# Optimization experiments

Measured on AMD Instinct MI355X. Metric: run time of the kernel, lower is better.

## Reference

```python
import jax, jax.numpy as jnp
import numpy as np

WIDTH = [768, 2048, 2048, 512]
GRID = 8
BATCH = 4096


def _init_coeffs(key, outdim, inputdim, gridsize):
    # smooth_initialization=True: randn / (sqrt(inputdim) * (k+1)^2)
    grid_norm = (jnp.arange(gridsize, dtype=jnp.float32) + 1.0) ** 2  # (grid,)
    c = jax.random.normal(key, (2, outdim, inputdim, gridsize), dtype=jnp.float32)
    return c / (np.sqrt(inputdim).astype(np.float32) * grid_norm)


def setup_inputs() -> dict:
    key = jax.random.key(0)
    ks = jax.random.split(key, 1 + len(WIDTH) - 1)
    x = jax.random.normal(ks[0], (BATCH, WIDTH[0]), dtype=jnp.float32)
    inp = {"x": x}
    for li, (din, dout) in enumerate(zip(WIDTH[:-1], WIDTH[1:])):
        inp[f"C{li + 1}"] = _init_coeffs(ks[li + 1], dout, din, GRID)
        inp[f"b{li + 1}"] = jnp.zeros((1, dout), dtype=jnp.float32)
    return inp


def _kan_layer(x, C, b):
    # x: (B, in); C: (2, out, in, grid); b: (1, out)
    g = C.shape[-1]
    k = jnp.arange(1, g + 1, dtype=x.dtype)  # (grid,)
    ang = x[..., None] * k  # (B, in, grid)
    feats = jnp.stack([jnp.cos(ang), jnp.sin(ang)], axis=0)  # (2, B, in, grid)
    # GEMM-like contraction over (in, grid) and the cos/sin axis
    y = jnp.einsum("dbik,djik->bj", feats, C) + b  # (B, out)
    return y


def reference(x, C1, b1, C2, b2, C3, b3):
    y = _kan_layer(x, C1, b1)
    y = _kan_layer(y, C2, b2)
    y = _kan_layer(y, C3, b3)
    return y
```

## Files before the change

kernel.cpp:

```cpp
#include <hip/hip_runtime.h>

#define BATCH 4096

typedef __attribute__((ext_vector_type(8))) short bf16x8;
typedef __attribute__((ext_vector_type(4))) float f32x4;

__device__ __forceinline__ unsigned short f2bf(float f) {
    union { float f; unsigned u; } v; v.f = f;
    unsigned r = v.u + 0x7fffu + ((v.u >> 16) & 1u);
    return (unsigned short)(r >> 16);
}
__device__ __forceinline__ unsigned packbf(float a, float b) {
    return (unsigned)f2bf(a) | ((unsigned)f2bf(b) << 16);
}

__device__ __forceinline__ void feats16(float x, unsigned o[8]) {
    float c1 = __cosf(x), s1 = __sinf(x);
    float cs[8], sn[8];
    cs[0] = c1; sn[0] = s1;
    #pragma unroll
    for (int k = 1; k < 8; ++k) {
        cs[k] = c1 * cs[k-1] - s1 * sn[k-1];
        sn[k] = s1 * cs[k-1] + c1 * sn[k-1];
    }
    #pragma unroll
    for (int k = 0; k < 4; ++k) {
        o[k]     = packbf(cs[2*k], cs[2*k+1]);
        o[4 + k] = packbf(sn[2*k], sn[2*k+1]);
    }
}

__device__ __forceinline__ void gload_lds16(const void* g, void* l) {
    __builtin_amdgcn_global_load_lds(
        (__attribute__((address_space(1))) void*)(g),
        (__attribute__((address_space(3))) void*)(l), 16, 0, 0);
}


template <int IN, int OUT>
__global__ void conv_C(const float* __restrict__ C, unsigned short* __restrict__ B) {
    const int i = blockIdx.x * 256 + threadIdx.x;
    const int j = blockIdx.y;
    const float* c0 = C + ((size_t)j * IN + i) * 8;
    const float* c1 = c0 + (size_t)OUT * IN * 8;
    const float4 a0 = *(const float4*)c0;
    const float4 a1 = *(const float4*)(c0 + 4);
    const float4 s0 = *(const float4*)c1;
    const float4 s1 = *(const float4*)(c1 + 4);
    unsigned short* dst = B + ((size_t)j * IN + i) * 16;
    *(uint4*)dst       = make_uint4(packbf(a0.x, a0.y), packbf(a0.z, a0.w),
                                    packbf(a1.x, a1.y), packbf(a1.z, a1.w));
    *(uint4*)(dst + 8) = make_uint4(packbf(s0.x, s0.y), packbf(s0.z, s0.w),
                                    packbf(s1.x, s1.y), packbf(s1.z, s1.w));
}

__global__ void feats_x_kernel(const float* __restrict__ x, unsigned short* __restrict__ A) {
    const size_t idx = (size_t)blockIdx.x * 256 + threadIdx.x;
    unsigned o[8];
    feats16(x[idx], o);
    unsigned short* dst = A + idx * 16;
    *(uint4*)dst       = make_uint4(o[0], o[1], o[2], o[3]);
    *(uint4*)(dst + 8) = make_uint4(o[4], o[5], o[6], o[7]);
}

template <int N, int KSPLIT>
__global__ void reduce_feats(const float* __restrict__ P, const float* __restrict__ bias,
                             unsigned short* __restrict__ A) {
    const size_t idx = (size_t)blockIdx.x * 256 + threadIdx.x;
    float s = P[idx];
    #pragma unroll
    for (int z = 1; z < KSPLIT; ++z) s += P[(size_t)z * BATCH * N + idx];
    s += bias[idx % N];
    unsigned o[8];
    feats16(s, o);
    unsigned short* dst = A + idx * 16;
    *(uint4*)dst       = make_uint4(o[0], o[1], o[2], o[3]);
    *(uint4*)(dst + 8) = make_uint4(o[4], o[5], o[6], o[7]);
}

template <int N, int KSPLIT>
__global__ void reduce_out(const float* __restrict__ P, const float* __restrict__ bias,
                           float* __restrict__ out) {
    const size_t idx = ((size_t)blockIdx.x * 256 + threadIdx.x) * 4;
    const int j = (int)(idx % N);
    float4 s = *(const float4*)(P + idx);
    #pragma unroll
    for (int z = 1; z < KSPLIT; ++z) {
        const float4 v = *(const float4*)(P + (size_t)z * BATCH * N + idx);
        s.x += v.x; s.y += v.y; s.z += v.z; s.w += v.w;
    }
    const float4 bv = *(const float4*)(bias + j);
    s.x += bv.x; s.y += bv.y; s.z += bv.z; s.w += bv.w;
    *(float4*)(out + idx) = s;
}

template <int K, int N, int KSPLIT>
__global__ __launch_bounds__(512, 2)
void kan_gemm(const unsigned short* __restrict__ A,
              const unsigned short* __restrict__ B,
              float* __restrict__ P)
{
    __shared__ unsigned short As[2 * 2 * 128 * 64];
    __shared__ unsigned short Bs[2 * 2 * 128 * 64];

    const int tid  = threadIdx.x;
    const int lane = tid & 63;
    const int wave = tid >> 6;
    const int wm   = wave >> 2;
    const int wn   = wave & 3;
    const int fr   = lane & 15;
    const int fq   = lane >> 4;

    constexpr int NBX = BATCH / 256;
    constexpr int NBY = N / 256;
    constexpr int NWG = NBX * NBY;
    constexpr int S   = NWG / 8;
    constexpr int CC  = (NBY >= 8) ? 8 : NBY;
    constexpr int CR  = S / CC;
    constexpr int GR  = NBX / CR;
    const int wg  = blockIdx.y * NBX + blockIdx.x;
    const int xc  = wg & 7;
    const int ci  = wg >> 3;
    const int row0 = ((xc % GR) * CR + ci % CR) * 256;
    const int col0 = ((xc / GR) * CC + ci / CR) * 256;

    constexpr int KCH = K / KSPLIT;
    const int kt0 = ((int)blockIdx.z * KCH) >> 6;
    const int nt  = KCH >> 6;

    const int srow = lane >> 3;
    const int scol = ((lane & 7) ^ srow) * 16;

    auto STA = [&](int b, int h, int kt) {
        #pragma unroll
        for (int r2 = 0; r2 < 2; ++r2)
            gload_lds16((const char*)A +
                        ((size_t)(row0 + h * 128 + r2 * 64 + wave * 8 + srow) * K + (size_t)kt * 64) * 2 + scol,
                        (char*)&As[((b * 2 + h) * 128 + r2 * 64 + wave * 8) * 64]);
    };
    auto STB = [&](int b, int h, int kt) {
        #pragma unroll
        for (int r2 = 0; r2 < 2; ++r2)
            gload_lds16((const char*)B +
                        ((size_t)(col0 + h * 128 + r2 * 64 + wave * 8 + srow) * K + (size_t)kt * 64) * 2 + scol,
                        (char*)&Bs[((b * 2 + h) * 128 + r2 * 64 + wave * 8) * 64]);
    };
    auto LDA = [&](int b, int m, int ks) -> bf16x8 {
        return *(const bf16x8*)&As[((b * 2 + wm) * 128 + m * 16 + fr) * 64 +
                                   (((ks * 4 + fq) ^ (fr & 7)) << 3)];
    };
    auto LDB = [&](int b, int n, int ks) -> bf16x8 {
        return *(const bf16x8*)&Bs[((b * 2 + (wn >> 1)) * 128 + (wn & 1) * 64 + n * 16 + fr) * 64 +
                                   (((ks * 4 + fq) ^ (fr & 7)) << 3)];
    };

    f32x4 acc[8][4] = {};

    STA(0, 0, kt0); STA(0, 1, kt0); STB(0, 0, kt0); STB(0, 1, kt0);
    STA(1, 0, kt0 + 1); STA(1, 1, kt0 + 1); STB(1, 0, kt0 + 1);
    asm volatile("s_waitcnt vmcnt(6)" ::: "memory");
    __builtin_amdgcn_s_barrier();

    #pragma unroll 1
    for (int t = 0; t < nt; ++t) {
        const int b  = t & 1;
        const int kt = kt0 + t;
        bf16x8 bF[8], aFa[8], aFb[8];

        #pragma unroll
        for (int n = 0; n < 4; ++n) { bF[n * 2] = LDB(b, n, 0); bF[n * 2 + 1] = LDB(b, n, 1); }
        #pragma unroll
        for (int mm = 0; mm < 4; ++mm) { aFa[mm * 2] = LDA(b, mm, 0); aFa[mm * 2 + 1] = LDA(b, mm, 1); }
        if (t + 1 < nt) STB(b ^ 1, 1, kt + 1);
        __builtin_amdgcn_s_barrier();
        asm volatile("s_waitcnt lgkmcnt(0)" ::: "memory");
        __builtin_amdgcn_sched_barrier(0);
        __builtin_amdgcn_s_setprio(1);
        #pragma unroll
        for (int ks = 0; ks < 2; ++ks)
            #pragma unroll
            for (int mm = 0; mm < 2; ++mm)
                #pragma unroll
                for (int n = 0; n < 4; ++n)
                    acc[mm][n] = __builtin_amdgcn_mfma_f32_16x16x32_bf16(
                        aFa[mm * 2 + ks], bF[n * 2 + ks], acc[mm][n], 0, 0, 0);
        __builtin_amdgcn_s_setprio(0);
        __builtin_amdgcn_s_barrier();

        #pragma unroll
        for (int mm = 0; mm < 4; ++mm) { aFb[mm * 2] = LDA(b, 4 + mm, 0); aFb[mm * 2 + 1] = LDA(b, 4 + mm, 1); }
        if (t + 2 < nt) STB(b, 0, kt + 2);
        __builtin_amdgcn_s_barrier();
        asm volatile("s_waitcnt lgkmcnt(0)" ::: "memory");
        __builtin_amdgcn_sched_barrier(0);
        __builtin_amdgcn_s_setprio(1);
        #pragma unroll
        for (int ks = 0; ks < 2; ++ks)
            #pragma unroll
            for (int mm = 0; mm < 2; ++mm)
                #pragma unroll
                for (int n = 0; n < 4; ++n)
                    acc[2 + mm][n] = __builtin_amdgcn_mfma_f32_16x16x32_bf16(
                        aFa[(2 + mm) * 2 + ks], bF[n * 2 + ks], acc[2 + mm][n], 0, 0, 0);
        __builtin_amdgcn_s_setprio(0);
        __builtin_amdgcn_s_barrier();

        if (t + 2 < nt) STA(b, 0, kt + 2);
        __builtin_amdgcn_s_barrier();
        __builtin_amdgcn_sched_barrier(0);
        __builtin_amdgcn_s_setprio(1);
        #pragma unroll
        for (int ks = 0; ks < 2; ++ks)
            #pragma unroll
            for (int mm = 0; mm < 2; ++mm)
                #pragma unroll
                for (int n = 0; n < 4; ++n)
                    acc[4 + mm][n] = __builtin_amdgcn_mfma_f32_16x16x32_bf16(
                        aFb[mm * 2 + ks], bF[n * 2 + ks], acc[4 + mm][n], 0, 0, 0);
        __builtin_amdgcn_s_setprio(0);
        __builtin_amdgcn_s_barrier();

        if (t + 2 < nt) {
            STA(b, 1, kt + 2);
            asm volatile("s_waitcnt vmcnt(6)" ::: "memory");
        } else {
            asm volatile("s_waitcnt vmcnt(0)" ::: "memory");
        }
        __builtin_amdgcn_s_barrier();
        __builtin_amdgcn_sched_barrier(0);
        __builtin_amdgcn_s_setprio(1);
        #pragma unroll
        for (int ks = 0; ks < 2; ++ks)
            #pragma unroll
            for (int mm = 0; mm < 2; ++mm)
                #pragma unroll
                for (int n = 0; n < 4; ++n)
                    acc[6 + mm][n] = __builtin_amdgcn_mfma_f32_16x16x32_bf16(
                        aFb[(2 + mm) * 2 + ks], bF[n * 2 + ks], acc[6 + mm][n], 0, 0, 0);
        __builtin_amdgcn_s_setprio(0);
        __builtin_amdgcn_s_barrier();
    }

    float* Pz = P + (size_t)blockIdx.z * BATCH * N;
    #pragma unroll
    for (int m = 0; m < 8; ++m) {
        const int gr0 = row0 + wm * 128 + m * 16 + fq * 4;
        #pragma unroll
        for (int n = 0; n < 4; ++n) {
            const int gc = col0 + wn * 64 + n * 16 + fr;
            #pragma unroll
            for (int q = 0; q < 4; ++q)
                Pz[(size_t)(gr0 + q) * N + gc] = acc[m][n][q];
        }
    }
}

extern "C" void kernel_launch(void* const* d_in, const int* in_sizes, int n_in,
                              void* d_out, int out_size, void* d_ws, size_t ws_size,
                              hipStream_t stream) {
    (void)in_sizes; (void)n_in; (void)ws_size; (void)out_size;
    const float* x  = (const float*)d_in[0];
    const float* C1 = (const float*)d_in[1];
    const float* b1 = (const float*)d_in[2];
    const float* C2 = (const float*)d_in[3];
    const float* b2 = (const float*)d_in[4];
    const float* C3 = (const float*)d_in[5];
    const float* b3 = (const float*)d_in[6];
    float* out = (float*)d_out;

    char* ws = (char*)d_ws;
    const size_t SZ_A1  = (size_t)4096 * 12288 * 2;
    const size_t SZ_B1  = (size_t)2048 * 12288 * 2;
    const size_t SZ_P12 = (size_t)2 * 4096 * 2048 * 4;
    const size_t SZ_A2  = (size_t)4096 * 32768 * 2;
    unsigned short* A1 = (unsigned short*)(ws);
    unsigned short* B1 = (unsigned short*)(ws + SZ_A1);
    float*          P1 = (float*)(ws + SZ_A1 + SZ_B1);
    unsigned short* A2 = (unsigned short*)(ws + SZ_A1 + SZ_B1 + SZ_P12);
    unsigned short* B2 = (unsigned short*)(ws);
    float*          P2 = (float*)(ws + SZ_A1 + SZ_B1 + SZ_P12 + SZ_A2);
    unsigned short* A3 = (unsigned short*)(ws);
    unsigned short* B3 = (unsigned short*)(ws + SZ_A2);
    float*          P3 = (float*)(ws + SZ_A2 + (size_t)512 * 32768 * 2);

    conv_C<768, 2048><<<dim3(768 / 256, 2048), 256, 0, stream>>>(C1, B1);
    feats_x_kernel<<<dim3((4096 * 768) / 256), 256, 0, stream>>>(x, A1);
    kan_gemm<12288, 2048, 2><<<dim3(16, 8, 2), 512, 0, stream>>>(A1, B1, P1);
    reduce_feats<2048, 2><<<dim3((BATCH * 2048) / 256), 256, 0, stream>>>(P1, b1, A2);

    conv_C<2048, 2048><<<dim3(2048 / 256, 2048), 256, 0, stream>>>(C2, B2);
    kan_gemm<32768, 2048, 2><<<dim3(16, 8, 2), 512, 0, stream>>>(A2, B2, P2);
    reduce_feats<2048, 2><<<dim3((BATCH * 2048) / 256), 256, 0, stream>>>(P2, b2, A3);

    conv_C<2048, 512><<<dim3(2048 / 256, 512), 256, 0, stream>>>(C3, B3);
    kan_gemm<32768, 512, 8><<<dim3(16, 2, 8), 512, 0, stream>>>(A3, B3, P3);
    reduce_out<512, 8><<<dim3((BATCH * 512 / 4) / 256), 256, 0, stream>>>(P3, b3, out);
}
```

Baseline: 1.147 ms.

## Software-pipeline LDS fragment loads across MFMA phases with partial lgkmcnt waits

Restructures the GEMM main loop so LDS fragment loads for the next phase are issued before the current MFMA phase. Partial lgkmcnt waits replace the full drains, and the first-k-slice fragments of the next tile are prefetched at the end of each tile. The loop is unrolled by two with a compile-time buffer index, and all three next-tile global stores are grouped into the last phase. The goal is to hide LDS read latency behind MFMA work. In exchange it needs more registers for carried fragments, and it assumes nt is even.

```diff
diff --git a/kernel.cpp b/kernel.cpp
--- a/kernel.cpp
+++ b/kernel.cpp
@@ -94,6 +94,9 @@
     *(float4*)(out + idx) = s;
 }
 
+struct IC0 { static constexpr int value = 0; };
+struct IC1 { static constexpr int value = 1; };
+
 template <int K, int N, int KSPLIT>
 __global__ __launch_bounds__(512, 2)
 void kan_gemm(const unsigned short* __restrict__ A,
@@ -155,90 +158,105 @@
     };
 
     f32x4 acc[8][4] = {};
+    bf16x8 cB0[4], cA0[4];
 
     STA(0, 0, kt0); STA(0, 1, kt0); STB(0, 0, kt0); STB(0, 1, kt0);
-    STA(1, 0, kt0 + 1); STA(1, 1, kt0 + 1); STB(1, 0, kt0 + 1);
+    STB(1, 0, kt0 + 1); STA(1, 0, kt0 + 1); STA(1, 1, kt0 + 1);
     asm volatile("s_waitcnt vmcnt(6)" ::: "memory");
+    __builtin_amdgcn_sched_barrier(0);
     __builtin_amdgcn_s_barrier();
-
-    #pragma unroll 1
-    for (int t = 0; t < nt; ++t) {
-        const int b  = t & 1;
+    #pragma unroll
+    for (int n = 0; n < 4; ++n) cB0[n] = LDB(0, n, 0);
+    #pragma unroll
+    for (int m = 0; m < 4; ++m) cA0[m] = LDA(0, m, 0);
+    __builtin_amdgcn_sched_barrier(0);
+
+    auto tile = [&](auto bc, int t) {
+        constexpr int b = decltype(bc)::value;
         const int kt = kt0 + t;
-        bf16x8 bF[8], aFa[8], aFb[8];
-
-        #pragma unroll
-        for (int n = 0; n < 4; ++n) { bF[n * 2] = LDB(b, n, 0); bF[n * 2 + 1] = LDB(b, n, 1); }
-        #pragma unroll
-        for (int mm = 0; mm < 4; ++mm) { aFa[mm * 2] = LDA(b, mm, 0); aFa[mm * 2 + 1] = LDA(b, mm, 1); }
+        bf16x8 vA01[4], vB1[4], vA10[4], vA11[4];
+
+        #pragma unroll
+        for (int m = 0; m < 4; ++m) vA01[m] = LDA(b, 4 + m, 0);
+        #pragma unroll
+        for (int n = 0; n < 4; ++n) vB1[n] = LDB(b, n, 1);
         if (t + 1 < nt) STB(b ^ 1, 1, kt + 1);
+        __builtin_amdgcn_sched_barrier(0);
+        __builtin_amdgcn_s_barrier();
+        asm volatile("s_waitcnt lgkmcnt(8)" ::: "memory");
+        __builtin_amdgcn_sched_barrier(0);
+        __builtin_amdgcn_s_setprio(1);
+        #pragma unroll
+        for (int m = 0; m < 4; ++m)
+            #pragma unroll
+            for (int n = 0; n < 4; ++n)
+                acc[m][n] = __builtin_amdgcn_mfma_f32_16x16x32_bf16(cA0[m], cB0[n], acc[m][n], 0, 0, 0);
+        __builtin_amdgcn_s_setprio(0);
+
+        #pragma unroll
+        for (int m = 0; m < 4; ++m) vA10[m] = LDA(b, m, 1);
+        #pragma unroll
+        for (int m = 0; m < 4; ++m) vA11[m] = LDA(b, 4 + m, 1);
+        __builtin_amdgcn_sched_barrier(0);
+        __builtin_amdgcn_s_barrier();
+        asm volatile("s_waitcnt lgkmcnt(12)" ::: "memory");
+        __builtin_amdgcn_sched_barrier(0);
+        __builtin_amdgcn_s_setprio(1);
+        #pragma unroll
+        for (int m = 0; m < 4; ++m)
+            #pragma unroll
+            for (int n = 0; n < 4; ++n)
+                acc[4 + m][n] = __builtin_amdgcn_mfma_f32_16x16x32_bf16(vA01[m], cB0[n], acc[4 + m][n], 0, 0, 0);
+        __builtin_amdgcn_s_setprio(0);
+
+        __builtin_amdgcn_sched_barrier(0);
         __builtin_amdgcn_s_barrier();
         asm volatile("s_waitcnt lgkmcnt(0)" ::: "memory");
         __builtin_amdgcn_sched_barrier(0);
         __builtin_amdgcn_s_setprio(1);
         #pragma unroll
-        for (int ks = 0; ks < 2; ++ks)
-            #pragma unroll
-            for (int mm = 0; mm < 2; ++mm)
-                #pragma unroll
-                for (int n = 0; n < 4; ++n)
-                    acc[mm][n] = __builtin_amdgcn_mfma_f32_16x16x32_bf16(
-                        aFa[mm * 2 + ks], bF[n * 2 + ks], acc[mm][n], 0, 0, 0);
+        for (int m = 0; m < 4; ++m)
+            #pragma unroll
+            for (int n = 0; n < 4; ++n)
+                acc[m][n] = __builtin_amdgcn_mfma_f32_16x16x32_bf16(vA10[m], vB1[n], acc[m][n], 0, 0, 0);
         __builtin_amdgcn_s_setprio(0);
-        __builtin_amdgcn_s_barrier();
-
-        #pragma unroll
-        for (int mm = 0; mm < 4; ++mm) { aFb[mm * 2] = LDA(b, 4 + mm, 0); aFb[mm * 2 + 1] = LDA(b, 4 + mm, 1); }
-        if (t + 2 < nt) STB(b, 0, kt + 2);
-        __builtin_amdgcn_s_barrier();
-        asm volatile("s_waitcnt lgkmcnt(0)" ::: "memory");
-        __builtin_amdgcn_sched_barrier(0);
-        __builtin_amdgcn_s_setprio(1);
-        #pragma unroll
-        for (int ks = 0; ks < 2; ++ks)
-            #pragma unroll
-            for (int mm = 0; mm < 2; ++mm)
-                #pragma unroll
-                for (int n = 0; n < 4; ++n)
-                    acc[2 + mm][n] = __builtin_amdgcn_mfma_f32_16x16x32_bf16(
-                        aFa[(2 + mm) * 2 + ks], bF[n * 2 + ks], acc[2 + mm][n], 0, 0, 0);
-        __builtin_amdgcn_s_setprio(0);
-        __builtin_amdgcn_s_barrier();
-
-        if (t + 2 < nt) STA(b, 0, kt + 2);
-        __builtin_amdgcn_s_barrier();
-        __builtin_amdgcn_sched_barrier(0);
-        __builtin_amdgcn_s_setprio(1);
-        #pragma unroll
-        for (int ks = 0; ks < 2; ++ks)
-            #pragma unroll
-            for (int mm = 0; mm < 2; ++mm)
-                #pragma unroll
-                for (int n = 0; n < 4; ++n)
-                    acc[4 + mm][n] = __builtin_amdgcn_mfma_f32_16x16x32_bf16(
-                        aFb[mm * 2 + ks], bF[n * 2 + ks], acc[4 + mm][n], 0, 0, 0);
-        __builtin_amdgcn_s_setprio(0);
+        __builtin_amdgcn_sched_barrier(0);
         __builtin_amdgcn_s_barrier();
 
         if (t + 2 < nt) {
-            STA(b, 1, kt + 2);
+            STB(b, 0, kt + 2); STA(b, 0, kt + 2); STA(b, 1, kt + 2);
             asm volatile("s_waitcnt vmcnt(6)" ::: "memory");
         } else {
             asm volatile("s_waitcnt vmcnt(0)" ::: "memory");
         }
-        __builtin_amdgcn_s_barrier();
+        __builtin_amdgcn_sched_barrier(0);
+        __builtin_amdgcn_s_barrier();
+        if (t + 1 < nt) {
+            #pragma unroll
+            for (int n = 0; n < 4; ++n) cB0[n] = LDB(b ^ 1, n, 0);
+            #pragma unroll
+            for (int m = 0; m < 4; ++m) cA0[m] = LDA(b ^ 1, m, 0);
+            __builtin_amdgcn_sched_barrier(0);
+            asm volatile("s_waitcnt lgkmcnt(8)" ::: "memory");
+        } else {
+            asm volatile("s_waitcnt lgkmcnt(0)" ::: "memory");
+        }
         __builtin_amdgcn_sched_barrier(0);
         __builtin_amdgcn_s_setprio(1);
         #pragma unroll
-        for (int ks = 0; ks < 2; ++ks)
-            #pragma unroll
-            for (int mm = 0; mm < 2; ++mm)
-                #pragma unroll
-                for (int n = 0; n < 4; ++n)
-                    acc[6 + mm][n] = __builtin_amdgcn_mfma_f32_16x16x32_bf16(
-                        aFb[(2 + mm) * 2 + ks], bF[n * 2 + ks], acc[6 + mm][n], 0, 0, 0);
+        for (int m = 0; m < 4; ++m)
+            #pragma unroll
+            for (int n = 0; n < 4; ++n)
+                acc[4 + m][n] = __builtin_amdgcn_mfma_f32_16x16x32_bf16(vA11[m], vB1[n], acc[4 + m][n], 0, 0, 0);
         __builtin_amdgcn_s_setprio(0);
-        __builtin_amdgcn_s_barrier();
+        __builtin_amdgcn_sched_barrier(0);
+        __builtin_amdgcn_s_barrier();
+    };
+
+    #pragma unroll 1
+    for (int t = 0; t < nt; t += 2) {
+        tile(IC0{}, t);
+        tile(IC1{}, t + 1);
     }
 
     float* Pz = P + (size_t)blockIdx.z * BATCH * N;
```

Result: slower. 3.355 ms (+192.6%).

## Relax GEMM LDS waits and barriers, vectorize reduce_feats by four

Applied to the files above, without the earlier changes.

The GEMM main loop drops the extra barrier after each MFMA phase. It replaces full lgkmcnt(0) waits with partial counts, so MFMAs can start while later LDS fragment reads are still in flight, and it adds sched_barriers to pin the instruction order. The reduce_feats kernel now handles four elements per thread with float4 loads and a quarter of the grid. Partial waits depend on the exact LDS instruction count and order, so any miscount or reordering could read stale fragments or race with the next buffer fill.

```diff
diff --git a/kernel.cpp b/kernel.cpp
--- a/kernel.cpp
+++ b/kernel.cpp
@@ -66,16 +66,24 @@
 template <int N, int KSPLIT>
 __global__ void reduce_feats(const float* __restrict__ P, const float* __restrict__ bias,
                              unsigned short* __restrict__ A) {
-    const size_t idx = (size_t)blockIdx.x * 256 + threadIdx.x;
-    float s = P[idx];
-    #pragma unroll
-    for (int z = 1; z < KSPLIT; ++z) s += P[(size_t)z * BATCH * N + idx];
-    s += bias[idx % N];
-    unsigned o[8];
-    feats16(s, o);
+    const size_t idx = ((size_t)blockIdx.x * 256 + threadIdx.x) * 4;
+    const int j = (int)(idx % N);
+    float4 s = *(const float4*)(P + idx);
+    #pragma unroll
+    for (int z = 1; z < KSPLIT; ++z) {
+        const float4 v = *(const float4*)(P + (size_t)z * BATCH * N + idx);
+        s.x += v.x; s.y += v.y; s.z += v.z; s.w += v.w;
+    }
+    const float4 bv = *(const float4*)(bias + j);
+    const float y[4] = { s.x + bv.x, s.y + bv.y, s.z + bv.z, s.w + bv.w };
     unsigned short* dst = A + idx * 16;
-    *(uint4*)dst       = make_uint4(o[0], o[1], o[2], o[3]);
-    *(uint4*)(dst + 8) = make_uint4(o[4], o[5], o[6], o[7]);
+    #pragma unroll
+    for (int e = 0; e < 4; ++e) {
+        unsigned o[8];
+        feats16(y[e], o);
+        *(uint4*)(dst + e * 16)     = make_uint4(o[0], o[1], o[2], o[3]);
+        *(uint4*)(dst + e * 16 + 8) = make_uint4(o[4], o[5], o[6], o[7]);
+    }
 }
 
 template <int N, int KSPLIT>
@@ -157,9 +165,10 @@
     f32x4 acc[8][4] = {};
 
     STA(0, 0, kt0); STA(0, 1, kt0); STB(0, 0, kt0); STB(0, 1, kt0);
-    STA(1, 0, kt0 + 1); STA(1, 1, kt0 + 1); STB(1, 0, kt0 + 1);
+    STB(1, 0, kt0 + 1); STA(1, 0, kt0 + 1); STA(1, 1, kt0 + 1);
     asm volatile("s_waitcnt vmcnt(6)" ::: "memory");
     __builtin_amdgcn_s_barrier();
+    __builtin_amdgcn_sched_barrier(0);
 
     #pragma unroll 1
     for (int t = 0; t < nt; ++t) {
@@ -170,10 +179,14 @@
         #pragma unroll
         for (int n = 0; n < 4; ++n) { bF[n * 2] = LDB(b, n, 0); bF[n * 2 + 1] = LDB(b, n, 1); }
         #pragma unroll
-        for (int mm = 0; mm < 4; ++mm) { aFa[mm * 2] = LDA(b, mm, 0); aFa[mm * 2 + 1] = LDA(b, mm, 1); }
+        for (int mm = 0; mm < 2; ++mm) { aFa[mm * 2] = LDA(b, mm, 0); aFa[mm * 2 + 1] = LDA(b, mm, 1); }
+        __builtin_amdgcn_sched_barrier(0);
+        #pragma unroll
+        for (int mm = 2; mm < 4; ++mm) { aFa[mm * 2] = LDA(b, mm, 0); aFa[mm * 2 + 1] = LDA(b, mm, 1); }
         if (t + 1 < nt) STB(b ^ 1, 1, kt + 1);
-        __builtin_amdgcn_s_barrier();
-        asm volatile("s_waitcnt lgkmcnt(0)" ::: "memory");
+        __builtin_amdgcn_sched_barrier(0);
+        __builtin_amdgcn_s_barrier();
+        asm volatile("s_waitcnt lgkmcnt(4)" ::: "memory");
         __builtin_amdgcn_sched_barrier(0);
         __builtin_amdgcn_s_setprio(1);
         #pragma unroll
@@ -185,13 +198,16 @@
                     acc[mm][n] = __builtin_amdgcn_mfma_f32_16x16x32_bf16(
                         aFa[mm * 2 + ks], bF[n * 2 + ks], acc[mm][n], 0, 0, 0);
         __builtin_amdgcn_s_setprio(0);
-        __builtin_amdgcn_s_barrier();
-
-        #pragma unroll
-        for (int mm = 0; mm < 4; ++mm) { aFb[mm * 2] = LDA(b, 4 + mm, 0); aFb[mm * 2 + 1] = LDA(b, 4 + mm, 1); }
+
+        #pragma unroll
+        for (int mm = 0; mm < 2; ++mm) { aFb[mm * 2] = LDA(b, 4 + mm, 0); aFb[mm * 2 + 1] = LDA(b, 4 + mm, 1); }
+        __builtin_amdgcn_sched_barrier(0);
+        #pragma unroll
+        for (int mm = 2; mm < 4; ++mm) { aFb[mm * 2] = LDA(b, 4 + mm, 0); aFb[mm * 2 + 1] = LDA(b, 4 + mm, 1); }
         if (t + 2 < nt) STB(b, 0, kt + 2);
-        __builtin_amdgcn_s_barrier();
-        asm volatile("s_waitcnt lgkmcnt(0)" ::: "memory");
+        __builtin_amdgcn_sched_barrier(0);
+        __builtin_amdgcn_s_barrier();
+        asm volatile("s_waitcnt lgkmcnt(8)" ::: "memory");
         __builtin_amdgcn_sched_barrier(0);
         __builtin_amdgcn_s_setprio(1);
         #pragma unroll
@@ -203,10 +219,11 @@
                     acc[2 + mm][n] = __builtin_amdgcn_mfma_f32_16x16x32_bf16(
                         aFa[(2 + mm) * 2 + ks], bF[n * 2 + ks], acc[2 + mm][n], 0, 0, 0);
         __builtin_amdgcn_s_setprio(0);
-        __builtin_amdgcn_s_barrier();
 
         if (t + 2 < nt) STA(b, 0, kt + 2);
-        __builtin_amdgcn_s_barrier();
+        __builtin_amdgcn_sched_barrier(0);
+        __builtin_amdgcn_s_barrier();
+        asm volatile("s_waitcnt lgkmcnt(4)" ::: "memory");
         __builtin_amdgcn_sched_barrier(0);
         __builtin_amdgcn_s_setprio(1);
         #pragma unroll
@@ -218,7 +235,6 @@
                     acc[4 + mm][n] = __builtin_amdgcn_mfma_f32_16x16x32_bf16(
                         aFb[mm * 2 + ks], bF[n * 2 + ks], acc[4 + mm][n], 0, 0, 0);
         __builtin_amdgcn_s_setprio(0);
-        __builtin_amdgcn_s_barrier();
 
         if (t + 2 < nt) {
             STA(b, 1, kt + 2);
@@ -226,7 +242,9 @@
         } else {
             asm volatile("s_waitcnt vmcnt(0)" ::: "memory");
         }
-        __builtin_amdgcn_s_barrier();
+        __builtin_amdgcn_sched_barrier(0);
+        __builtin_amdgcn_s_barrier();
+        asm volatile("s_waitcnt lgkmcnt(0)" ::: "memory");
         __builtin_amdgcn_sched_barrier(0);
         __builtin_amdgcn_s_setprio(1);
         #pragma unroll
@@ -238,6 +256,7 @@
                     acc[6 + mm][n] = __builtin_amdgcn_mfma_f32_16x16x32_bf16(
                         aFb[(2 + mm) * 2 + ks], bF[n * 2 + ks], acc[6 + mm][n], 0, 0, 0);
         __builtin_amdgcn_s_setprio(0);
+        __builtin_amdgcn_sched_barrier(0);
         __builtin_amdgcn_s_barrier();
     }
 
@@ -286,11 +305,11 @@
     conv_C<768, 2048><<<dim3(768 / 256, 2048), 256, 0, stream>>>(C1, B1);
     feats_x_kernel<<<dim3((4096 * 768) / 256), 256, 0, stream>>>(x, A1);
     kan_gemm<12288, 2048, 2><<<dim3(16, 8, 2), 512, 0, stream>>>(A1, B1, P1);
-    reduce_feats<2048, 2><<<dim3((BATCH * 2048) / 256), 256, 0, stream>>>(P1, b1, A2);
+    reduce_feats<2048, 2><<<dim3((BATCH * 2048 / 4) / 256), 256, 0, stream>>>(P1, b1, A2);
 
     conv_C<2048, 2048><<<dim3(2048 / 256, 2048), 256, 0, stream>>>(C2, B2);
     kan_gemm<32768, 2048, 2><<<dim3(16, 8, 2), 512, 0, stream>>>(A2, B2, P2);
-    reduce_feats<2048, 2><<<dim3((BATCH * 2048) / 256), 256, 0, stream>>>(P2, b2, A3);
+    reduce_feats<2048, 2><<<dim3((BATCH * 2048 / 4) / 256), 256, 0, stream>>>(P2, b2, A3);
 
     conv_C<2048, 512><<<dim3(2048 / 256, 512), 256, 0, stream>>>(C3, B3);
     kan_gemm<32768, 512, 8><<<dim3(16, 2, 8), 512, 0, stream>>>(A3, B3, P3);
```

Result: no change. 1.160 ms (median of 3 runs) (+1.2%).
